# Performance work log

Hardware: AMD Instinct MI355X
Metric: run time of the kernel (lower is better)

Reference implementation:

```python
import jax, jax.numpy as jnp
import numpy as np

N = 50000
E = 800000
IN_C, HID_C, OUT_C = 256, 128, 64


def setup_inputs() -> dict:
    key = jax.random.key(0)
    k1, k2, k3, k4 = jax.random.split(key, 4)
    x = jax.random.normal(k1, (N, IN_C), dtype=jnp.float32)
    edge_index = jax.random.randint(k2, (2, E), 0, N, dtype=jnp.int64)
    # Glorot-ish init for GCN weights, zero bias (PyG default)
    W1 = jax.random.normal(k3, (IN_C, HID_C), dtype=jnp.float32) / np.sqrt(IN_C)
    b1 = jnp.zeros((HID_C,), dtype=jnp.float32)
    W2 = jax.random.normal(k4, (HID_C, OUT_C), dtype=jnp.float32) / np.sqrt(HID_C)
    b2 = jnp.zeros((OUT_C,), dtype=jnp.float32)
    return {"x": x, "edge_index": edge_index, "W1": W1, "b1": b1, "W2": W2, "b2": b2}


def _gcn_norm(edge_index, num_nodes):
    # Add self-loops, compute symmetric normalization D^-1/2 A D^-1/2 (PyG GCNConv default)
    loops = jnp.arange(num_nodes, dtype=edge_index.dtype)
    src = jnp.concatenate([edge_index[0], loops])  # message sources
    dst = jnp.concatenate([edge_index[1], loops])  # aggregation targets
    deg = jax.ops.segment_sum(jnp.ones_like(dst, dtype=jnp.float32), dst,
                              num_segments=num_nodes)
    dinv = jnp.where(deg > 0, jax.lax.rsqrt(deg), 0.0)
    norm = dinv[src] * dinv[dst]  # [E+N]
    return src, dst, norm


def _gcn_conv(x, W, b, src, dst, norm, num_nodes):
    h = x @ W                                   # [N, out]
    msg = h[src] * norm[:, None]                # gather + scale, [E+N, out]
    out = jax.ops.segment_sum(msg, dst, num_segments=num_nodes)  # scatter-add
    return out + b


def reference(x, edge_index, W1, b1, W2, b2):
    num_nodes = x.shape[0]
    src, dst, norm = _gcn_norm(edge_index, num_nodes)
    h = _gcn_conv(x, W1, b1, src, dst, norm, num_nodes)
    h = jax.nn.relu(h)
    # F.dropout(training=False) -> identity at inference
    return _gcn_conv(h, W2, b2, src, dst, norm, num_nodes)
```

## Files before the change

### kernel.cpp

```cpp
#include <hip/hip_runtime.h>
#include <hip/hip_bf16.h>


typedef __attribute__((ext_vector_type(8))) short short8;
typedef __attribute__((ext_vector_type(4))) float f32x4;

union BF8 {
    short8 s;
    uint4 u;
    __hip_bfloat162 h[4];
};

__device__ __forceinline__ unsigned short f32_to_bf16_rne(float f) {
    unsigned u = __float_as_uint(f);
    return (unsigned short)((u + 0x7fffu + ((u >> 16) & 1u)) >> 16);
}
__device__ __forceinline__ float bf_lo(unsigned v) { return __uint_as_float(v << 16); }
__device__ __forceinline__ float bf_hi(unsigned v) { return __uint_as_float(v & 0xffff0000u); }

#define ACHUNK 16384
#define BSH 6
#define BN 64
#define CAP 2048

__global__ void wfrag_zero_kernel(const float* __restrict__ W1, const float* __restrict__ W2,
                                  unsigned short* __restrict__ w1f,
                                  unsigned short* __restrict__ w2f,
                                  int* __restrict__ counts, int* __restrict__ bcursor,
                                  int n, int nbk) {
    int i = blockIdx.x * blockDim.x + threadIdx.x;
    if (i < n) counts[i] = 0;
    if (i < nbk) bcursor[i] = 0;
    const float* W;
    unsigned short* WF;
    int KS, NCOL, idx;
    if (i < 32768) {
        W = W1; WF = w1f; KS = 8; NCOL = 128; idx = i;
    } else if (i < 32768 + 8192) {
        W = W2; WF = w2f; KS = 4; NCOL = 64; idx = i - 32768;
    } else return;
    int j = idx & 7;
    int lane = (idx >> 3) & 63;
    int f = idx >> 9;
    int ks = f % KS, nt = f / KS;
    int m16 = lane & 15, quad = lane >> 4;
    int ncol = nt * 16 + m16;
    int k = ks * 32 + quad * 8 + j;
    WF[idx] = f32_to_bf16_rne(W[k * NCOL + ncol]);
}

__global__ __launch_bounds__(256) void gemm1_bucket_kernel(
    const float* __restrict__ A, const unsigned short* __restrict__ BFRAG,
    unsigned short* __restrict__ C, int M, int gGemm,
    const int* __restrict__ src, const int* __restrict__ dst,
    int* __restrict__ counts, int* __restrict__ bcursor,
    int2* __restrict__ tmp, int e, int nbk) {
    constexpr int NT = 8, KS = 8;
    constexpr int K = KS * 32;
    constexpr int LSTRIDE = K + 8;
    __shared__ char smem[64 * LSTRIDE * 2];

    const int tid = threadIdx.x;
    if ((int)blockIdx.x < gGemm) {
        unsigned short* Alds = (unsigned short*)smem;
        const int wave = tid >> 6, lane = tid & 63;
        const int quad = lane >> 4, m16 = lane & 15;
        const int rowBase = blockIdx.x * 64;

        constexpr int HALVES = K / 128;
#pragma unroll
        for (int h = 0; h < HALVES; h++) {
            f32x4 v[8];
#pragma unroll
            for (int it = 0; it < 8; it++) {
                int p = (h * 8 + it) * 1024 + tid * 4;
                int rg = rowBase + p / K;
                if (rg >= M) rg = M - 1;
                v[it] = *(const f32x4*)(A + (size_t)rg * K + (p % K));
            }
#pragma unroll
            for (int it = 0; it < 8; it++) {
                int p = (h * 8 + it) * 1024 + tid * 4;
                BF8 cv;
                cv.h[0] = __float22bfloat162_rn(make_float2(v[it].x, v[it].y));
                cv.h[1] = __float22bfloat162_rn(make_float2(v[it].z, v[it].w));
                *(uint2*)&Alds[(p / K) * LSTRIDE + (p % K)] = make_uint2(cv.u.x, cv.u.y);
            }
        }
        __syncthreads();

        const unsigned short* Afrag0 = &Alds[(wave * 16 + m16) * LSTRIDE + quad * 8];
        const uint4* Bfrag = (const uint4*)BFRAG + lane;

        f32x4 acc[NT];
#pragma unroll
        for (int nt = 0; nt < NT; nt++) acc[nt] = f32x4{0.f, 0.f, 0.f, 0.f};
#pragma unroll
        for (int ks = 0; ks < KS; ks++) {
            BF8 af;
            af.u = *(const uint4*)(Afrag0 + ks * 32);
#pragma unroll
            for (int nt = 0; nt < NT; nt++) {
                BF8 bf;
                bf.u = Bfrag[(nt * KS + ks) * 64];
                acc[nt] = __builtin_amdgcn_mfma_f32_16x16x32_bf16(af.s, bf.s, acc[nt], 0, 0, 0);
            }
        }
        const int rowOut = rowBase + wave * 16 + quad * 4;
#pragma unroll
        for (int nt = 0; nt < NT; nt++) {
#pragma unroll
            for (int r = 0; r < 4; r++) {
                int row = rowOut + r;
                if (row < M)
                    C[(size_t)row * 128 + nt * 16 + m16] = f32_to_bf16_rne(acc[nt][r]);
            }
        }
    } else {
        int* hist = (int*)smem;
        int* base = hist + 1024;
        int* cur  = base + 1024;
        const int b0 = blockIdx.x - gGemm;
        const int start = b0 * ACHUNK;
        const int cnt = min(ACHUNK, e - start);
        for (int t = tid; t < nbk; t += 256) { hist[t] = 0; cur[t] = 0; }
        __syncthreads();
        for (int i = tid; i < cnt; i += 256) {
            int d = dst[start + i];
            atomicAdd(&counts[d], 1);
            atomicAdd(&hist[d >> BSH], 1);
        }
        __syncthreads();
        for (int t = tid; t < nbk; t += 256) {
            int h = hist[t];
            base[t] = (h > 0) ? atomicAdd(&bcursor[t], h) : 0;
        }
        __syncthreads();
        for (int i = tid; i < cnt; i += 256) {
            int d = dst[start + i];
            int s = src[start + i];
            int bk = d >> BSH;
            int slot = base[bk] + atomicAdd(&cur[bk], 1);
            if (slot < CAP)
                tmp[(size_t)bk * CAP + slot] = make_int2(s, d);
        }
    }
}

__global__ __launch_bounds__(256) void aggsort_gemm2_kernel(
    const int* __restrict__ counts, const int2* __restrict__ tmp,
    const int* __restrict__ bcursor,
    const unsigned short* __restrict__ hb,
    const float* __restrict__ bias1,
    const unsigned short* __restrict__ w2frag,
    int2* __restrict__ sedge, int2* __restrict__ nodeRange,
    unsigned short* __restrict__ h2, int n) {
    constexpr int LSTRIDE = 136;
    __shared__ int ecnt[BN];
    __shared__ int estart[BN];
    __shared__ int lcur[BN];
    __shared__ float ndinv[BN];
    __shared__ int ssrc[CAP];
    __shared__ float swt[CAP];
    __shared__ unsigned short a1lds[BN * LSTRIDE];

    const int tid = threadIdx.x;
    const int b = blockIdx.x;
    const int nodeBase = b << BSH;
    const int nNodes = min(BN, n - nodeBase);
    const int cnt = min(bcursor[b], CAP);

    if (tid < BN) ecnt[tid] = 0;
    __syncthreads();

    for (int i = tid; i < cnt; i += 256)
        atomicAdd(&ecnt[tmp[(size_t)b * CAP + i].y - nodeBase], 1);
    __syncthreads();

    if (tid < BN) {
        int c = ecnt[tid];
        int x = c;
#pragma unroll
        for (int off = 1; off < 64; off <<= 1) {
            int y = __shfl_up(x, off, 64);
            if (tid >= off) x += y;
        }
        int st = x - c;
        estart[tid] = st;
        lcur[tid] = st;
        ndinv[tid] = rsqrtf((float)c + 1.0f);
        if (tid < nNodes) nodeRange[nodeBase + tid] = make_int2(b * CAP + st, c);
    }
    __syncthreads();

    for (int i = tid; i < cnt; i += 256) {
        int2 r = tmp[(size_t)b * CAP + i];
        int ln = r.y - nodeBase;
        float w = rsqrtf((float)counts[r.x] + 1.0f) * ndinv[ln];
        int pos = atomicAdd(&lcur[ln], 1);
        ssrc[pos] = r.x;
        swt[pos] = w;
    }
    __syncthreads();
    for (int i = tid; i < cnt; i += 256)
        sedge[(size_t)b * CAP + i] = make_int2(ssrc[i], __float_as_int(swt[i]));

    const int sub = tid & 15;
    const int qw = tid >> 4;
    for (int pass = 0; pass < BN / 16; pass++) {
        int ln = pass * 16 + qw;
        float a0 = 0.f, a1 = 0.f, a2 = 0.f, a3 = 0.f;
        float a4 = 0.f, a5 = 0.f, a6 = 0.f, a7 = 0.f;
        if (ln < nNodes) {
            int node = nodeBase + ln;
            float di = ndinv[ln];
            float d2 = di * di;
            uint4 sv = ((const uint4*)(hb + (size_t)node * 128))[sub];
            a0 = d2 * bf_lo(sv.x); a1 = d2 * bf_hi(sv.x);
            a2 = d2 * bf_lo(sv.y); a3 = d2 * bf_hi(sv.y);
            a4 = d2 * bf_lo(sv.z); a5 = d2 * bf_hi(sv.z);
            a6 = d2 * bf_lo(sv.w); a7 = d2 * bf_hi(sv.w);
            int beg = estart[ln];
            int end = beg + ecnt[ln];
            int i = beg;
            for (; i + 8 <= end; i += 8) {
                int s[8]; float w[8]; uint4 v[8];
#pragma unroll
                for (int j = 0; j < 8; j++) { s[j] = ssrc[i + j]; w[j] = swt[i + j]; }
#pragma unroll
                for (int j = 0; j < 8; j++)
                    v[j] = ((const uint4*)(hb + (size_t)s[j] * 128))[sub];
#pragma unroll
                for (int j = 0; j < 8; j++) {
                    a0 = fmaf(w[j], bf_lo(v[j].x), a0); a1 = fmaf(w[j], bf_hi(v[j].x), a1);
                    a2 = fmaf(w[j], bf_lo(v[j].y), a2); a3 = fmaf(w[j], bf_hi(v[j].y), a3);
                    a4 = fmaf(w[j], bf_lo(v[j].z), a4); a5 = fmaf(w[j], bf_hi(v[j].z), a5);
                    a6 = fmaf(w[j], bf_lo(v[j].w), a6); a7 = fmaf(w[j], bf_hi(v[j].w), a7);
                }
            }
            for (; i + 4 <= end; i += 4) {
                int s[4]; float w[4]; uint4 v[4];
#pragma unroll
                for (int j = 0; j < 4; j++) { s[j] = ssrc[i + j]; w[j] = swt[i + j]; }
#pragma unroll
                for (int j = 0; j < 4; j++)
                    v[j] = ((const uint4*)(hb + (size_t)s[j] * 128))[sub];
#pragma unroll
                for (int j = 0; j < 4; j++) {
                    a0 = fmaf(w[j], bf_lo(v[j].x), a0); a1 = fmaf(w[j], bf_hi(v[j].x), a1);
                    a2 = fmaf(w[j], bf_lo(v[j].y), a2); a3 = fmaf(w[j], bf_hi(v[j].y), a3);
                    a4 = fmaf(w[j], bf_lo(v[j].z), a4); a5 = fmaf(w[j], bf_hi(v[j].z), a5);
                    a6 = fmaf(w[j], bf_lo(v[j].w), a6); a7 = fmaf(w[j], bf_hi(v[j].w), a7);
                }
            }
            for (; i < end; ++i) {
                int s = ssrc[i];
                float w = swt[i];
                uint4 v = ((const uint4*)(hb + (size_t)s * 128))[sub];
                a0 = fmaf(w, bf_lo(v.x), a0); a1 = fmaf(w, bf_hi(v.x), a1);
                a2 = fmaf(w, bf_lo(v.y), a2); a3 = fmaf(w, bf_hi(v.y), a3);
                a4 = fmaf(w, bf_lo(v.z), a4); a5 = fmaf(w, bf_hi(v.z), a5);
                a6 = fmaf(w, bf_lo(v.w), a6); a7 = fmaf(w, bf_hi(v.w), a7);
            }
            float4 b0v = ((const float4*)bias1)[sub * 2];
            float4 b1v = ((const float4*)bias1)[sub * 2 + 1];
            a0 = fmaxf(a0 + b0v.x, 0.f); a1 = fmaxf(a1 + b0v.y, 0.f);
            a2 = fmaxf(a2 + b0v.z, 0.f); a3 = fmaxf(a3 + b0v.w, 0.f);
            a4 = fmaxf(a4 + b1v.x, 0.f); a5 = fmaxf(a5 + b1v.y, 0.f);
            a6 = fmaxf(a6 + b1v.z, 0.f); a7 = fmaxf(a7 + b1v.w, 0.f);
        }
        BF8 p;
        p.h[0] = __float22bfloat162_rn(make_float2(a0, a1));
        p.h[1] = __float22bfloat162_rn(make_float2(a2, a3));
        p.h[2] = __float22bfloat162_rn(make_float2(a4, a5));
        p.h[3] = __float22bfloat162_rn(make_float2(a6, a7));
        *(uint4*)&a1lds[ln * LSTRIDE + sub * 8] = p.u;
    }
    __syncthreads();

    const int wave = tid >> 6, lane = tid & 63;
    const int quad = lane >> 4, m16 = lane & 15;
    const unsigned short* Afrag0 = &a1lds[(wave * 16 + m16) * LSTRIDE + quad * 8];
    const uint4* Bfrag = (const uint4*)w2frag + lane;

    f32x4 acc[4];
#pragma unroll
    for (int nt = 0; nt < 4; nt++) acc[nt] = f32x4{0.f, 0.f, 0.f, 0.f};
#pragma unroll
    for (int ks = 0; ks < 4; ks++) {
        BF8 af;
        af.u = *(const uint4*)(Afrag0 + ks * 32);
#pragma unroll
        for (int nt = 0; nt < 4; nt++) {
            BF8 bf;
            bf.u = Bfrag[(nt * 4 + ks) * 64];
            acc[nt] = __builtin_amdgcn_mfma_f32_16x16x32_bf16(af.s, bf.s, acc[nt], 0, 0, 0);
        }
    }
    const int rowOut = wave * 16 + quad * 4;
#pragma unroll
    for (int nt = 0; nt < 4; nt++) {
#pragma unroll
        for (int r = 0; r < 4; r++) {
            int row = rowOut + r;
            if (row < nNodes)
                h2[(size_t)(nodeBase + row) * 64 + nt * 16 + m16] =
                    f32_to_bf16_rne(acc[nt][r]);
        }
    }
}

__global__ __launch_bounds__(256, 8) void agg64_kernel(
    const int2* __restrict__ nodeRange, const int2* __restrict__ sedge,
    const unsigned short* __restrict__ hb,
    const float* __restrict__ bias, float* __restrict__ out, int n) {
    int node = blockIdx.x * 16 + (threadIdx.x >> 4);
    if (node >= n) return;
    int sub = threadIdx.x & 15;
    int2 nr = nodeRange[node];
    float di = rsqrtf((float)nr.y + 1.0f);
    float d2 = di * di;
    uint2 sv = ((const uint2*)(hb + (size_t)node * 64))[sub];
    float a0 = d2 * bf_lo(sv.x), a1 = d2 * bf_hi(sv.x);
    float a2 = d2 * bf_lo(sv.y), a3 = d2 * bf_hi(sv.y);
    int beg = nr.x, end = nr.x + nr.y;
    int i = beg;
    for (; i + 8 <= end; i += 8) {
        int2 e[8];
        uint2 v[8];
#pragma unroll
        for (int j = 0; j < 8; j++) e[j] = sedge[i + j];
#pragma unroll
        for (int j = 0; j < 8; j++)
            v[j] = ((const uint2*)(hb + (size_t)e[j].x * 64))[sub];
#pragma unroll
        for (int j = 0; j < 8; j++) {
            float w = __int_as_float(e[j].y);
            a0 = fmaf(w, bf_lo(v[j].x), a0); a1 = fmaf(w, bf_hi(v[j].x), a1);
            a2 = fmaf(w, bf_lo(v[j].y), a2); a3 = fmaf(w, bf_hi(v[j].y), a3);
        }
    }
    for (; i + 4 <= end; i += 4) {
        int2 e[4];
        uint2 v[4];
#pragma unroll
        for (int j = 0; j < 4; j++) e[j] = sedge[i + j];
#pragma unroll
        for (int j = 0; j < 4; j++)
            v[j] = ((const uint2*)(hb + (size_t)e[j].x * 64))[sub];
#pragma unroll
        for (int j = 0; j < 4; j++) {
            float w = __int_as_float(e[j].y);
            a0 = fmaf(w, bf_lo(v[j].x), a0); a1 = fmaf(w, bf_hi(v[j].x), a1);
            a2 = fmaf(w, bf_lo(v[j].y), a2); a3 = fmaf(w, bf_hi(v[j].y), a3);
        }
    }
    for (; i < end; ++i) {
        int2 e = sedge[i];
        float w = __int_as_float(e.y);
        uint2 v = ((const uint2*)(hb + (size_t)e.x * 64))[sub];
        a0 = fmaf(w, bf_lo(v.x), a0); a1 = fmaf(w, bf_hi(v.x), a1);
        a2 = fmaf(w, bf_lo(v.y), a2); a3 = fmaf(w, bf_hi(v.y), a3);
    }
    float4 bv = ((const float4*)bias)[sub];
    ((float4*)(out + (size_t)node * 64))[sub] =
        make_float4(a0 + bv.x, a1 + bv.y, a2 + bv.z, a3 + bv.w);
}

extern "C" void kernel_launch(void* const* d_in, const int* in_sizes, int n_in,
                              void* d_out, int out_size, void* d_ws, size_t ws_size,
                              hipStream_t stream) {
    const float* x  = (const float*)d_in[0];
    const int*   ei = (const int*)d_in[1];
    const float* W1 = (const float*)d_in[2];
    const float* b1 = (const float*)d_in[3];
    const float* W2 = (const float*)d_in[4];
    const float* b2 = (const float*)d_in[5];
    float* out = (float*)d_out;

    const int IN_C = 256;
    const int N = in_sizes[0] / IN_C;
    const int E = in_sizes[1] / 2;
    const int* srcA = ei;
    const int* dstA = ei + E;

    char* ws = (char*)d_ws;
    const size_t KB = 1024, MB = 1024 * 1024;
    int*            counts    = (int*)(ws);
    int*            bcursor   = (int*)(ws + 256 * KB);
    unsigned short* w1f       = (unsigned short*)(ws + 1 * MB);
    unsigned short* w2f       = (unsigned short*)(ws + 1 * MB + 64 * KB);
    int2*           tmp       = (int2*)(ws + 2 * MB);
    int2*           sedge     = (int2*)(ws + 16 * MB);
    int2*           nodeRange = (int2*)(ws + 30 * MB);
    unsigned short* h1b       = (unsigned short*)(ws + 31 * MB);
    unsigned short* h2b       = (unsigned short*)(ws + 44 * MB);

    const int NB = (N + BN - 1) / BN;
    const int gGemm = (N + 63) / 64;
    const int nbA = (E + ACHUNK - 1) / ACHUNK;
    const int gWfrag = (max(N, 32768 + 8192) + 255) / 256;

    wfrag_zero_kernel<<<gWfrag, 256, 0, stream>>>(W1, W2, w1f, w2f, counts, bcursor, N, NB);
    gemm1_bucket_kernel<<<gGemm + nbA, 256, 0, stream>>>(
        x, w1f, h1b, N, gGemm, srcA, dstA, counts, bcursor, tmp, E, NB);
    aggsort_gemm2_kernel<<<NB, 256, 0, stream>>>(
        counts, tmp, bcursor, h1b, b1, w2f, sedge, nodeRange, h2b, N);
    agg64_kernel<<<(N + 15) / 16, 256, 0, stream>>>(nodeRange, sedge, h2b, b2, out, N);
}
```

Baseline: 227.0 us.

## Shrink bucketing chunks, cache dst in LDS, drop LDS edge staging in aggregation

The bucketing phase now processes 2048-edge chunks instead of 16384, so many more blocks run it. Destination indices are cached in shared memory, and the separate cursor array is dropped by reusing the histogram as the running slot counter. In the aggregation/GEMM2 kernel the per-block ssrc/swt shared arrays (16KB) are removed: sorted edges go straight to global sedge and are read back from there. Launch bounds request 8 blocks per CU to raise occupancy, at the cost of global re-reads of edge data and more global atomics on bcursor.

```diff
diff --git a/kernel.cpp b/kernel.cpp
--- a/kernel.cpp
+++ b/kernel.cpp
@@ -18,7 +18,7 @@
 __device__ __forceinline__ float bf_lo(unsigned v) { return __uint_as_float(v << 16); }
 __device__ __forceinline__ float bf_hi(unsigned v) { return __uint_as_float(v & 0xffff0000u); }
 
-#define ACHUNK 16384
+#define ACHUNK 2048
 #define BSH 6
 #define BN 64
 #define CAP 2048
@@ -117,37 +117,35 @@
             }
         }
     } else {
-        int* hist = (int*)smem;
-        int* base = hist + 1024;
-        int* cur  = base + 1024;
+        int* sdst = (int*)smem;
+        int* hist = (int*)((char*)smem + ACHUNK * 4);
         const int b0 = blockIdx.x - gGemm;
         const int start = b0 * ACHUNK;
         const int cnt = min(ACHUNK, e - start);
-        for (int t = tid; t < nbk; t += 256) { hist[t] = 0; cur[t] = 0; }
+        for (int t = tid; t < nbk; t += 256) hist[t] = 0;
         __syncthreads();
         for (int i = tid; i < cnt; i += 256) {
             int d = dst[start + i];
+            sdst[i] = d;
             atomicAdd(&counts[d], 1);
             atomicAdd(&hist[d >> BSH], 1);
         }
         __syncthreads();
         for (int t = tid; t < nbk; t += 256) {
             int h = hist[t];
-            base[t] = (h > 0) ? atomicAdd(&bcursor[t], h) : 0;
+            hist[t] = (h > 0) ? atomicAdd(&bcursor[t], h) : 0;
         }
         __syncthreads();
         for (int i = tid; i < cnt; i += 256) {
-            int d = dst[start + i];
-            int s = src[start + i];
-            int bk = d >> BSH;
-            int slot = base[bk] + atomicAdd(&cur[bk], 1);
-            if (slot < CAP)
-                tmp[(size_t)bk * CAP + slot] = make_int2(s, d);
-        }
-    }
-}
-
-__global__ __launch_bounds__(256) void aggsort_gemm2_kernel(
+            int d = sdst[i];
+            int slot = atomicAdd(&hist[d >> BSH], 1);
+            if ((unsigned)slot < (unsigned)CAP)
+                tmp[(size_t)(d >> BSH) * CAP + slot] = make_int2(src[start + i], d);
+        }
+    }
+}
+
+__global__ __launch_bounds__(256, 8) void aggsort_gemm2_kernel(
     const int* __restrict__ counts, const int2* __restrict__ tmp,
     const int* __restrict__ bcursor,
     const unsigned short* __restrict__ hb,
@@ -160,8 +158,6 @@
     __shared__ int estart[BN];
     __shared__ int lcur[BN];
     __shared__ float ndinv[BN];
-    __shared__ int ssrc[CAP];
-    __shared__ float swt[CAP];
     __shared__ unsigned short a1lds[BN * LSTRIDE];
 
     const int tid = threadIdx.x;
@@ -198,12 +194,9 @@
         int ln = r.y - nodeBase;
         float w = rsqrtf((float)counts[r.x] + 1.0f) * ndinv[ln];
         int pos = atomicAdd(&lcur[ln], 1);
-        ssrc[pos] = r.x;
-        swt[pos] = w;
-    }
-    __syncthreads();
-    for (int i = tid; i < cnt; i += 256)
-        sedge[(size_t)b * CAP + i] = make_int2(ssrc[i], __float_as_int(swt[i]));
+        sedge[(size_t)b * CAP + pos] = make_int2(r.x, __float_as_int(w));
+    }
+    __syncthreads();
 
     const int sub = tid & 15;
     const int qw = tid >> 4;
@@ -220,43 +213,30 @@
             a2 = d2 * bf_lo(sv.y); a3 = d2 * bf_hi(sv.y);
             a4 = d2 * bf_lo(sv.z); a5 = d2 * bf_hi(sv.z);
             a6 = d2 * bf_lo(sv.w); a7 = d2 * bf_hi(sv.w);
+            const int2* seg = sedge + (size_t)b * CAP;
             int beg = estart[ln];
             int end = beg + ecnt[ln];
             int i = beg;
-            for (; i + 8 <= end; i += 8) {
-                int s[8]; float w[8]; uint4 v[8];
-#pragma unroll
-                for (int j = 0; j < 8; j++) { s[j] = ssrc[i + j]; w[j] = swt[i + j]; }
-#pragma unroll
-                for (int j = 0; j < 8; j++)
-                    v[j] = ((const uint4*)(hb + (size_t)s[j] * 128))[sub];
-#pragma unroll
-                for (int j = 0; j < 8; j++) {
-                    a0 = fmaf(w[j], bf_lo(v[j].x), a0); a1 = fmaf(w[j], bf_hi(v[j].x), a1);
-                    a2 = fmaf(w[j], bf_lo(v[j].y), a2); a3 = fmaf(w[j], bf_hi(v[j].y), a3);
-                    a4 = fmaf(w[j], bf_lo(v[j].z), a4); a5 = fmaf(w[j], bf_hi(v[j].z), a5);
-                    a6 = fmaf(w[j], bf_lo(v[j].w), a6); a7 = fmaf(w[j], bf_hi(v[j].w), a7);
+            for (; i + 4 <= end; i += 4) {
+                int2 e[4]; uint4 v[4];
+#pragma unroll
+                for (int j = 0; j < 4; j++) e[j] = seg[i + j];
+#pragma unroll
+                for (int j = 0; j < 4; j++)
+                    v[j] = ((const uint4*)(hb + (size_t)e[j].x * 128))[sub];
+#pragma unroll
+                for (int j = 0; j < 4; j++) {
+                    float w = __int_as_float(e[j].y);
+                    a0 = fmaf(w, bf_lo(v[j].x), a0); a1 = fmaf(w, bf_hi(v[j].x), a1);
+                    a2 = fmaf(w, bf_lo(v[j].y), a2); a3 = fmaf(w, bf_hi(v[j].y), a3);
+                    a4 = fmaf(w, bf_lo(v[j].z), a4); a5 = fmaf(w, bf_hi(v[j].z), a5);
+                    a6 = fmaf(w, bf_lo(v[j].w), a6); a7 = fmaf(w, bf_hi(v[j].w), a7);
                 }
             }
-            for (; i + 4 <= end; i += 4) {
-                int s[4]; float w[4]; uint4 v[4];
-#pragma unroll
-                for (int j = 0; j < 4; j++) { s[j] = ssrc[i + j]; w[j] = swt[i + j]; }
-#pragma unroll
-                for (int j = 0; j < 4; j++)
-                    v[j] = ((const uint4*)(hb + (size_t)s[j] * 128))[sub];
-#pragma unroll
-                for (int j = 0; j < 4; j++) {
-                    a0 = fmaf(w[j], bf_lo(v[j].x), a0); a1 = fmaf(w[j], bf_hi(v[j].x), a1);
-                    a2 = fmaf(w[j], bf_lo(v[j].y), a2); a3 = fmaf(w[j], bf_hi(v[j].y), a3);
-                    a4 = fmaf(w[j], bf_lo(v[j].z), a4); a5 = fmaf(w[j], bf_hi(v[j].z), a5);
-                    a6 = fmaf(w[j], bf_lo(v[j].w), a6); a7 = fmaf(w[j], bf_hi(v[j].w), a7);
-                }
-            }
             for (; i < end; ++i) {
-                int s = ssrc[i];
-                float w = swt[i];
-                uint4 v = ((const uint4*)(hb + (size_t)s * 128))[sub];
+                int2 e = seg[i];
+                float w = __int_as_float(e.y);
+                uint4 v = ((const uint4*)(hb + (size_t)e.x * 128))[sub];
                 a0 = fmaf(w, bf_lo(v.x), a0); a1 = fmaf(w, bf_hi(v.x), a1);
                 a2 = fmaf(w, bf_lo(v.y), a2); a3 = fmaf(w, bf_hi(v.y), a3);
                 a4 = fmaf(w, bf_lo(v.z), a4); a5 = fmaf(w, bf_hi(v.z), a5);
```

Result: faster. 208.0 us (-8.4%).
